# Optimization experiments

Hardware: AMD Instinct MI355X
Metric: run time of the kernel (lower is better)

The kernel has to match this reference:

```python
import jax, jax.numpy as jnp
import numpy as np

N_HEADS = 16
DIM = 1024
BS, SLEN = 2, 2048
EPS = 1e-12  # F.normalize eps


def setup_inputs() -> dict:
    key = jax.random.key(0)
    ks = jax.random.split(key, 10)
    d = DIM
    inp = {
        "x": jax.random.normal(ks[0], (BS, SLEN, d), dtype=jnp.float32),
        # causal attention mask, as produced by get_masks(causal=True)
        "mask": jnp.tril(jnp.ones((SLEN, SLEN), dtype=bool))[None].repeat(BS, axis=0),
        "Wq": jax.random.normal(ks[1], (d, d), dtype=jnp.float32) / np.sqrt(d),
        "bq": jax.random.normal(ks[2], (d,), dtype=jnp.float32) * 0.02,
        "Wk": jax.random.normal(ks[3], (d, d), dtype=jnp.float32) / np.sqrt(d),
        "bk": jax.random.normal(ks[4], (d,), dtype=jnp.float32) * 0.02,
        "Wv": jax.random.normal(ks[5], (d, d), dtype=jnp.float32) / np.sqrt(d),
        "bv": jax.random.normal(ks[6], (d,), dtype=jnp.float32) * 0.02,
        "Wo": jax.random.normal(ks[7], (d, d), dtype=jnp.float32) / np.sqrt(d),
        "bo": jax.random.normal(ks[8], (d,), dtype=jnp.float32) * 0.02,
        # learnable scale for normalized (cosine) attention
        "attention_scale": jnp.ones((1,), dtype=jnp.float32) / np.sqrt(d // N_HEADS),
    }
    return inp


def _shape(t, bs, h, dph):
    # (bs, len, dim) -> (bs, h, len, dph)
    return t.reshape(bs, -1, h, dph).transpose(0, 2, 1, 3)


def reference(x, mask, Wq, bq, Wk, bk, Wv, bv, Wo, bo, attention_scale):
    bs, qlen, dim = x.shape
    h = N_HEADS
    dph = dim // h

    q = _shape(x @ Wq + bq, bs, h, dph)  # (bs, h, qlen, dph)
    k = _shape(x @ Wk + bk, bs, h, dph)
    v = _shape(x @ Wv + bv, bs, h, dph)

    # normalized (cosine) attention: L2-normalize q and k, learned scale
    q = q / jnp.maximum(jnp.linalg.norm(q, axis=-1, keepdims=True), EPS)
    k = k / jnp.maximum(jnp.linalg.norm(k, axis=-1, keepdims=True), EPS)
    q = q * attention_scale

    scores = jnp.einsum("bhqd,bhkd->bhqk", q, k)  # (bs, h, qlen, klen)
    scores = jnp.where(mask[:, None, :, :], scores, -jnp.inf)
    weights = jax.nn.softmax(scores, axis=-1)

    ctx = jnp.einsum("bhqk,bhkd->bhqd", weights, v)
    ctx = ctx.transpose(0, 2, 1, 3).reshape(bs, qlen, dim)
    return ctx @ Wo + bo
```

## Files before the change

### kernel.cpp

```cpp
#include <hip/hip_runtime.h>
#include <math.h>

#define NH 16
#define DPH 64
#define SLEN 2048
#define BSZ 2
#define DIM 1024
#define NTOK (BSZ * SLEN)
#define LOG2E 1.44269504088896f

typedef unsigned short ushortT;
typedef __attribute__((ext_vector_type(8))) short short8;
typedef __attribute__((ext_vector_type(4))) float f32x4;

typedef __attribute__((address_space(1))) const unsigned int gu32c;
typedef __attribute__((address_space(3))) unsigned int lu32;

__device__ __forceinline__ void gld16(const void* g, void* l) {
    __builtin_amdgcn_global_load_lds((gu32c*)g, (lu32*)l, 16, 0, 0);
}

__device__ __forceinline__ ushortT f2bf(float f) {
    unsigned int u = __builtin_bit_cast(unsigned int, f);
    u = u + 0x7fffu + ((u >> 16) & 1u);
    return (ushortT)(u >> 16);
}

__device__ __forceinline__ unsigned int cvtpk_bf16(float a, float b) {
    unsigned int r;
    asm("v_cvt_pk_bf16_f32 %0, %1, %2" : "=v"(r) : "v"(a), "v"(b));
    return r;
}

__global__ __launch_bounds__(256) void cvt_all(const float* __restrict__ x,
                                               ushortT* __restrict__ xb,
                                               const float* __restrict__ W0, const float* __restrict__ W1,
                                               const float* __restrict__ W2, const float* __restrict__ W3,
                                               ushortT* __restrict__ T0, ushortT* __restrict__ T1,
                                               ushortT* __restrict__ T2, ushortT* __restrict__ T3) {
    __shared__ float tile[64][65];
    const int tid = threadIdx.x;
    const int bid = blockIdx.x;
    if (bid < 2048) {
        size_t i = (size_t)bid * 256 + tid;
        float4 a = *(const float4*)&x[i * 8];
        float4 b = *(const float4*)&x[i * 8 + 4];
        short8 v;
        v[0] = (short)f2bf(a.x); v[1] = (short)f2bf(a.y);
        v[2] = (short)f2bf(a.z); v[3] = (short)f2bf(a.w);
        v[4] = (short)f2bf(b.x); v[5] = (short)f2bf(b.y);
        v[6] = (short)f2bf(b.z); v[7] = (short)f2bf(b.w);
        *(short8*)&xb[i * 8] = v;
        return;
    }
    const int widx = bid - 2048;
    const int z = widx >> 8, rem = widx & 255;
    const float* W = z == 0 ? W0 : z == 1 ? W1 : z == 2 ? W2 : W3;
    ushortT* T = z == 0 ? T0 : z == 1 ? T1 : z == 2 ? T2 : T3;
    const int kb = (rem >> 4) * 64, nb = (rem & 15) * 64;
#pragma unroll
    for (int it = 0; it < 4; it++) {
        int chunk = it * 256 + tid;
        int r = chunk >> 4, c4 = (chunk & 15) * 4;
        *(float4*)&tile[r][c4] = *(const float4*)&W[(size_t)(kb + r) * DIM + nb + c4];
    }
    __syncthreads();
#pragma unroll
    for (int it = 0; it < 2; it++) {
        int chunk = it * 256 + tid;
        int n = chunk >> 3, k8 = (chunk & 7) * 8;
        short8 o;
#pragma unroll
        for (int j = 0; j < 8; j++) o[j] = (short)f2bf(tile[k8 + j][n]);
        *(short8*)&T[(size_t)(nb + n) * DIM + kb + k8] = o;
    }
}

__global__ __launch_bounds__(1024, 4) void gemm_qkv8(const ushortT* __restrict__ A,
                                                     const ushortT* __restrict__ Bt,
                                                     const float* __restrict__ bq,
                                                     const float* __restrict__ bk,
                                                     const float* __restrict__ bv,
                                                     const float* __restrict__ ascale,
                                                     ushortT* __restrict__ Qb,
                                                     ushortT* __restrict__ Kb,
                                                     ushortT* __restrict__ VF) {
    __shared__ __align__(16) ushortT lds[65536];
    const int tid = threadIdx.x;
    const int lane = tid & 63, wid = tid >> 6;
    const int wm = wid >> 2, wn = wid & 3;
    const int lo = lane & 15, hi = lane >> 4;
    const int bid = blockIdx.x;
    const int swz = (bid & 7) * 24 + (bid >> 3);
    const int bx = swz % 12, by = swz / 12;
    const int row0 = by * 256, col0 = bx * 256;
    const int srow = tid >> 2, sc = tid & 3;
    f32x4 acc[4][4] = {};
    short8 af[4], bfr[4];

    auto stage = [&](int isA, int buf, int ksh, int kt) {
        const ushortT* g = isA ? A : Bt;
        int r0 = isA ? row0 : col0;
        int base = (isA ? 0 : 32768) + (buf * 2 + ksh) * 8192;
        int gch = sc ^ ((srow >> 1) & 3);
        gld16(&g[(size_t)(r0 + srow) * DIM + kt * 64 + ksh * 32 + gch * 8],
              &lds[base + tid * 8]);
    };
    auto loadA = [&](int buf, int ks) {
        int base = (buf * 2 + ks) * 8192;
#pragma unroll
        for (int mm = 0; mm < 4; mm++) {
            int row = wm * 64 + mm * 16 + lo;
            af[mm] = *(const short8*)&lds[base + row * 32 + (hi ^ ((row >> 1) & 3)) * 8];
        }
    };
    auto loadB = [&](int buf, int ks) {
        int base = 32768 + (buf * 2 + ks) * 8192;
#pragma unroll
        for (int n = 0; n < 4; n++) {
            int row = wn * 64 + n * 16 + lo;
            bfr[n] = *(const short8*)&lds[base + row * 32 + (hi ^ ((row >> 1) & 3)) * 8];
        }
    };
    auto mfma16 = [&]() {
        __builtin_amdgcn_s_setprio(1);
#pragma unroll
        for (int mm = 0; mm < 4; mm++)
#pragma unroll
            for (int n = 0; n < 4; n++)
                acc[mm][n] = __builtin_amdgcn_mfma_f32_16x16x32_bf16(
                    af[mm], bfr[n], acc[mm][n], 0, 0, 0);
        __builtin_amdgcn_s_setprio(0);
    };

    stage(0, 0, 0, 0); stage(1, 0, 0, 0);
    stage(0, 0, 1, 0); stage(1, 0, 1, 0);

#pragma unroll 1
    for (int t = 0; t < 16; ++t) {
        const int cur = t & 1, nxt = cur ^ 1;
        const bool more = (t < 15);
        asm volatile("s_waitcnt vmcnt(0)" ::: "memory");
        asm volatile("s_barrier" ::: "memory");
        loadA(cur, 0); loadB(cur, 0);
        if (more) { stage(0, nxt, 0, t + 1); stage(1, nxt, 0, t + 1); }
        mfma16();
        loadA(cur, 1); loadB(cur, 1);
        if (more) { stage(0, nxt, 1, t + 1); stage(1, nxt, 1, t + 1); }
        mfma16();
    }
    __syncthreads();

    const int cg = col0 + wn * 64;
    const int which = cg >> 10;
    const int cwin = cg & 1023;
    const int h = cwin >> 6;
    const int t0g = row0 + wm * 64;
    const int b = t0g >> 11, tok0 = t0g & (SLEN - 1);
    const float* bias = which == 0 ? bq : which == 1 ? bk : bv;

    float bb4[4];
#pragma unroll
    for (int n = 0; n < 4; n++) bb4[n] = bias[cwin + n * 16 + lo];
#pragma unroll
    for (int m = 0; m < 4; m++)
#pragma unroll
        for (int n = 0; n < 4; n++)
#pragma unroll
            for (int r = 0; r < 4; r++) acc[m][n][r] += bb4[n];

    if (which < 2) {
        float asc = (which == 0) ? ascale[0] * LOG2E : 1.0f;
#pragma unroll
        for (int m = 0; m < 4; m++)
#pragma unroll
            for (int r = 0; r < 4; r++) {
                float ss = acc[m][0][r] * acc[m][0][r] + acc[m][1][r] * acc[m][1][r] +
                           acc[m][2][r] * acc[m][2][r] + acc[m][3][r] * acc[m][3][r];
#pragma unroll
                for (int o = 8; o > 0; o >>= 1) ss += __shfl_xor(ss, o);
                float sc2 = asc / fmaxf(sqrtf(ss), 1e-12f);
#pragma unroll
                for (int n = 0; n < 4; n++) acc[m][n][r] *= sc2;
            }
    }

    ushortT* tl = &lds[wid * 4096];
    if (which < 2) {
#pragma unroll
        for (int m = 0; m < 4; m++)
#pragma unroll
            for (int n = 0; n < 4; n++)
#pragma unroll
                for (int r = 0; r < 4; r++) {
                    int row = m * 16 + 4 * hi + r;
                    int c = n * 2 + (lo >> 3);
                    tl[row * 64 + ((c ^ (row & 7)) << 3) + (lo & 7)] = f2bf(acc[m][n][r]);
                }
        ushortT* op = which == 0 ? Qb : Kb;
        const size_t base = ((size_t)(b * NH + h) * SLEN + tok0) * DPH;
#pragma unroll
        for (int j = 0; j < 8; j++) {
            int cid = j * 64 + lane;
            int rowL = cid >> 3, c = cid & 7;
            uint4 v = *(const uint4*)&tl[rowL * 64 + ((c ^ (rowL & 7)) << 3)];
            *(uint4*)&op[base + (size_t)cid * 8] = v;
        }
    } else {
#pragma unroll
        for (int m = 0; m < 4; m++)
#pragma unroll
            for (int n = 0; n < 4; n++)
#pragma unroll
                for (int r = 0; r < 4; r++) {
                    int row = m * 16 + 4 * hi + r;
                    int c = n * 2 + (lo >> 3);
                    tl[row * 64 + ((c ^ ((row >> 3) & 7)) << 3) + (lo & 7)] = f2bf(acc[m][n][r]);
                }
        const int bh = b * NH + h;
        const int kt = tok0 >> 6;
#pragma unroll
        for (int c2i = 0; c2i < 8; c2i++) {
            int jd = c2i >> 1, ks2 = c2i & 1;
            int colL = jd * 16 + lo;
            int cc2 = colL >> 3;
            short8 v;
#pragma unroll
            for (int e = 0; e < 8; e++) {
                int rowL = ks2 * 32 + 8 * hi + e;
                v[e] = (short)tl[rowL * 64 + ((cc2 ^ ((rowL >> 3) & 7)) << 3) + (colL & 7)];
            }
            *(short8*)&VF[((size_t)bh * 32 + kt) * 4096 + (size_t)(c2i * 64 + lane) * 8] = v;
        }
    }
}

__global__ __launch_bounds__(512, 2) void gemm_oproj(const ushortT* __restrict__ A,
                                                     const ushortT* __restrict__ Bt,
                                                     const float* __restrict__ bias,
                                                     float* __restrict__ outF) {
    __shared__ __align__(16) ushortT lds[32768];
    const int tid = threadIdx.x;
    const int lane = tid & 63, wid = tid >> 6;
    const int wm = wid >> 2, wn = wid & 3;
    const int lo = lane & 15, hi = lane >> 4;
    const int bid = blockIdx.x;
    const int swz = (bid & 7) * 32 + (bid >> 3);
    const int bx = swz & 7, by = swz >> 3;
    const int row0 = by * 128, col0 = bx * 128;
    const int srow = tid >> 2, sc = tid & 3;
    f32x4 acc[4][2] = {};
    short8 afO[2], bfO[2];

    auto stage = [&](int isA, int buf, int ksh, int kt) {
        const ushortT* g = isA ? A : Bt;
        int r0 = isA ? row0 : col0;
        int base = (isA ? 0 : 16384) + (buf * 2 + ksh) * 4096;
        int gch = sc ^ ((srow >> 1) & 3);
        gld16(&g[(size_t)(r0 + srow) * DIM + kt * 64 + ksh * 32 + gch * 8],
              &lds[base + tid * 8]);
    };
    auto loadAO = [&](int buf, int ks, int mh) {
        int base = (buf * 2 + ks) * 4096;
#pragma unroll
        for (int mm = 0; mm < 2; mm++) {
            int row = wm * 64 + (mh * 2 + mm) * 16 + lo;
            afO[mm] = *(const short8*)&lds[base + row * 32 + (hi ^ ((row >> 1) & 3)) * 8];
        }
    };
    auto loadBO = [&](int buf, int ks) {
        int base = 16384 + (buf * 2 + ks) * 4096;
#pragma unroll
        for (int n = 0; n < 2; n++) {
            int row = wn * 32 + n * 16 + lo;
            bfO[n] = *(const short8*)&lds[base + row * 32 + (hi ^ ((row >> 1) & 3)) * 8];
        }
    };
    auto mfma4 = [&](int mh) {
        __builtin_amdgcn_s_setprio(1);
#pragma unroll
        for (int mm = 0; mm < 2; mm++)
#pragma unroll
            for (int n = 0; n < 2; n++)
                acc[mh * 2 + mm][n] = __builtin_amdgcn_mfma_f32_16x16x32_bf16(
                    afO[mm], bfO[n], acc[mh * 2 + mm][n], 0, 0, 0);
        __builtin_amdgcn_s_setprio(0);
    };

    stage(1, 0, 0, 0); stage(0, 0, 0, 0);
    stage(1, 0, 1, 0); stage(0, 0, 1, 0);
    stage(1, 1, 0, 1); stage(0, 1, 0, 1);

#pragma unroll 1
    for (int it = 0; it < 8; ++it) {
        const int o = it * 2 + 1;
        const bool more = (it < 7);
        asm volatile("s_waitcnt vmcnt(4)" ::: "memory");
        asm volatile("s_barrier" ::: "memory");
        loadAO(0, 0, 0); loadBO(0, 0);
        stage(1, 1, 1, o);
        mfma4(0);
        asm volatile("s_barrier" ::: "memory");
        loadAO(0, 0, 1);
        stage(0, 1, 1, o);
        mfma4(1);
        asm volatile("s_waitcnt vmcnt(4)" ::: "memory");
        asm volatile("s_barrier" ::: "memory");
        loadAO(0, 1, 0); loadBO(0, 1);
        if (more) stage(1, 0, 0, o + 1);
        mfma4(0);
        asm volatile("s_barrier" ::: "memory");
        loadAO(0, 1, 1);
        if (more) stage(0, 0, 0, o + 1);
        mfma4(1);
        if (more) { asm volatile("s_waitcnt vmcnt(4)" ::: "memory"); }
        else      { asm volatile("s_waitcnt vmcnt(2)" ::: "memory"); }
        asm volatile("s_barrier" ::: "memory");
        loadAO(1, 0, 0); loadBO(1, 0);
        if (more) stage(1, 0, 1, o + 1);
        mfma4(0);
        asm volatile("s_barrier" ::: "memory");
        loadAO(1, 0, 1);
        if (more) stage(0, 0, 1, o + 1);
        mfma4(1);
        if (more) { asm volatile("s_waitcnt vmcnt(4)" ::: "memory"); }
        else      { asm volatile("s_waitcnt vmcnt(0)" ::: "memory"); }
        asm volatile("s_barrier" ::: "memory");
        loadAO(1, 1, 0); loadBO(1, 1);
        if (more) stage(1, 1, 0, o + 2);
        mfma4(0);
        asm volatile("s_barrier" ::: "memory");
        loadAO(1, 1, 1);
        if (more) stage(0, 1, 0, o + 2);
        mfma4(1);
    }
    __syncthreads();

    float bb[2];
#pragma unroll
    for (int n = 0; n < 2; n++) bb[n] = bias[col0 + wn * 32 + n * 16 + lo];
#pragma unroll
    for (int m = 0; m < 4; m++)
#pragma unroll
        for (int n = 0; n < 2; n++)
#pragma unroll
            for (int r = 0; r < 4; r++) acc[m][n][r] += bb[n];

    float* tl = (float*)&lds[wid * 4096];
#pragma unroll
    for (int m = 0; m < 4; m++)
#pragma unroll
        for (int n = 0; n < 2; n++)
#pragma unroll
            for (int r = 0; r < 4; r++) {
                int row = m * 16 + hi * 4 + r;
                int col = n * 16 + lo;
                int cc = col >> 2;
                tl[row * 32 + ((cc ^ (row & 7)) << 2) + (col & 3)] = acc[m][n][r];
            }
#pragma unroll
    for (int j = 0; j < 8; j++) {
        int cid = j * 64 + lane;
        int rowR = cid >> 3, cc = cid & 7;
        f32x4 v = *(const f32x4*)&tl[rowR * 32 + ((cc ^ (rowR & 7)) << 2)];
        int rg = row0 + wm * 64 + rowR;
        int cgl = col0 + wn * 32 + cc * 4;
        *(f32x4*)&outF[(size_t)rg * DIM + cgl] = v;
    }
}

__global__ __launch_bounds__(512, 4) void attn(const ushortT* __restrict__ Q,
                                               const ushortT* __restrict__ K,
                                               const ushortT* __restrict__ VF,
                                               const float* __restrict__ scale,
                                               ushortT* __restrict__ ctx) {
    __shared__ __align__(16) ushortT Ks[2][64 * 64];
    __shared__ __align__(16) ushortT Ps[8 * 16 * 64];
    const int tid = threadIdx.x, lane = tid & 63, wid = tid >> 6;
    const int wg = wid & 3, sg = wid >> 2;
    const int bh = blockIdx.x, p = blockIdx.y;
    const int qt = sg ? p : 31 - p;
    const int kbmax = 31 - p;
    const size_t hb = (size_t)bh * SLEN * DPH;
    const int lo = lane & 15, hi = lane >> 4;
    const float mshift = fabsf(scale[0]) * LOG2E;

    short8 aq[2];
    {
        const int qrow = qt * 64 + wg * 16 + lo;
#pragma unroll
        for (int ks = 0; ks < 2; ks++)
            aq[ks] = *(const short8*)&Q[hb + (size_t)qrow * DPH + ks * 32 + 8 * hi];
    }

    const int srow = tid >> 3, sslot = tid & 7;
    const int sldsoff = srow * 64 + ((sslot ^ (srow & 7)) << 3);
    uint4 kr = *(const uint4*)&K[hb + (size_t)srow * DPH + sslot * 8];
    *(uint4*)&Ks[0][sldsoff] = kr;
    __syncthreads();

    f32x4 accd[4] = {};
    float lp = 0.f;

    for (int kb = 0; kb <= kbmax; kb++) {
        const int cur = kb & 1;
        if (kb < kbmax)
            kr = *(const uint4*)&K[hb + (size_t)((kb + 1) * 64 + srow) * DPH + sslot * 8];

        if (kb <= qt) {
            short8 bv[8];
            const ushortT* vt = &VF[(((size_t)bh * 32 + kb) * 512 + lane) * 8];
#pragma unroll
            for (int c = 0; c < 8; c++) bv[c] = *(const short8*)&vt[(size_t)c * 512];

            f32x4 sf[4] = {};
            __builtin_amdgcn_s_setprio(1);
#pragma unroll
            for (int ks = 0; ks < 2; ks++)
#pragma unroll
                for (int j = 0; j < 4; j++) {
                    int row = j * 16 + lo;
                    short8 bk = *(const short8*)&Ks[cur][row * 64 + (((ks * 4 + hi) ^ (row & 7)) << 3)];
                    sf[j] = __builtin_amdgcn_mfma_f32_16x16x32_bf16(bk, aq[ks], sf[j], 0, 0, 0);
                }
            __builtin_amdgcn_s_setprio(0);

            if (kb == qt) {
#pragma unroll
                for (int j = 0; j < 4; j++)
#pragma unroll
                    for (int r = 0; r < 4; r++)
                        if (j * 16 + 4 * hi + r > wg * 16 + lo) sf[j][r] = -INFINITY;
            }

#pragma unroll
            for (int j = 0; j < 4; j++) {
                float pv0 = __builtin_amdgcn_exp2f(sf[j][0] - mshift);
                float pv1 = __builtin_amdgcn_exp2f(sf[j][1] - mshift);
                float pv2 = __builtin_amdgcn_exp2f(sf[j][2] - mshift);
                float pv3 = __builtin_amdgcn_exp2f(sf[j][3] - mshift);
                lp += (pv0 + pv1) + (pv2 + pv3);
                uint2 pk;
                pk.x = cvtpk_bf16(pv0, pv1);
                pk.y = cvtpk_bf16(pv2, pv3);
                int slot = (4 * j + hi) ^ (2 * (lo & 7));
                *(uint2*)&Ps[wid * 1024 + lo * 64 + slot * 4] = pk;
            }

            __builtin_amdgcn_s_setprio(1);
#pragma unroll
            for (int ks = 0; ks < 2; ks++) {
                int slot0 = (8 * ks + 2 * hi) ^ (2 * (lo & 7));
                short8 ap = *(const short8*)&Ps[wid * 1024 + lo * 64 + slot0 * 4];
#pragma unroll
                for (int jd = 0; jd < 4; jd++)
                    accd[jd] = __builtin_amdgcn_mfma_f32_16x16x32_bf16(ap, bv[jd * 2 + ks], accd[jd], 0, 0, 0);
            }
            __builtin_amdgcn_s_setprio(0);
        }

        if (kb < kbmax) *(uint4*)&Ks[cur ^ 1][sldsoff] = kr;
        __syncthreads();
    }

    lp += __shfl_xor(lp, 16);
    lp += __shfl_xor(lp, 32);

    const int b = bh >> 4, h = bh & 15;
#pragma unroll
    for (int r = 0; r < 4; r++) {
        float lr = __shfl(lp, (lane & 48) | (4 * hi + r));
        float inv = 1.0f / lr;
        int t = qt * 64 + wg * 16 + 4 * hi + r;
#pragma unroll
        for (int jd = 0; jd < 4; jd++) {
            int d = jd * 16 + lo;
            ctx[(size_t)(b * SLEN + t) * DIM + h * 64 + d] = f2bf(accd[jd][r] * inv);
        }
    }
}

extern "C" void kernel_launch(void* const* d_in, const int* in_sizes, int n_in,
                              void* d_out, int out_size, void* d_ws,
                              size_t ws_size, hipStream_t stream) {
    const float* x = (const float*)d_in[0];
    const float* Wq = (const float*)d_in[2];
    const float* bq = (const float*)d_in[3];
    const float* Wk = (const float*)d_in[4];
    const float* bk = (const float*)d_in[5];
    const float* Wv = (const float*)d_in[6];
    const float* bv = (const float*)d_in[7];
    const float* Wo = (const float*)d_in[8];
    const float* bo = (const float*)d_in[9];
    const float* ascale = (const float*)d_in[10];
    float* outF = (float*)d_out;

    unsigned char* ws = (unsigned char*)d_ws;
    const size_t MB = 1u << 20;
    ushortT* xb = (ushortT*)(ws);
    ushortT* Wqkvt = (ushortT*)(ws + 8 * MB);
    ushortT* Wot = (ushortT*)(ws + 14 * MB);
    ushortT* Qb = (ushortT*)(ws + 16 * MB);
    ushortT* Kb = (ushortT*)(ws + 24 * MB);
    ushortT* VFb = (ushortT*)(ws + 32 * MB);
    ushortT* ctxb = (ushortT*)(ws + 40 * MB);

    cvt_all<<<3072, 256, 0, stream>>>(x, xb, Wq, Wk, Wv, Wo, Wqkvt,
                                      Wqkvt + (size_t)1024 * 1024,
                                      Wqkvt + (size_t)2048 * 1024, Wot);

    gemm_qkv8<<<dim3(192), 1024, 0, stream>>>(xb, Wqkvt, bq, bk, bv, ascale, Qb, Kb, VFb);

    attn<<<dim3(32, 16), 512, 0, stream>>>(Qb, Kb, VFb, ascale, ctxb);

    gemm_oproj<<<dim3(256), 512, 0, stream>>>(ctxb, Wot, bo, outF);
}
```

Measured before the change: 91.42 us.

## Simplify oproj GEMM to double-buffered loop and rebalance attention tile pairing

```diff
diff --git a/kernel.cpp b/kernel.cpp
--- a/kernel.cpp
+++ b/kernel.cpp
@@ -287,51 +287,24 @@
         __builtin_amdgcn_s_setprio(0);
     };
 
-    stage(1, 0, 0, 0); stage(0, 0, 0, 0);
-    stage(1, 0, 1, 0); stage(0, 0, 1, 0);
-    stage(1, 1, 0, 1); stage(0, 1, 0, 1);
+    stage(0, 0, 0, 0); stage(1, 0, 0, 0);
+    stage(0, 0, 1, 0); stage(1, 0, 1, 0);
 
 #pragma unroll 1
-    for (int it = 0; it < 8; ++it) {
-        const int o = it * 2 + 1;
-        const bool more = (it < 7);
-        asm volatile("s_waitcnt vmcnt(4)" ::: "memory");
+    for (int t = 0; t < 16; ++t) {
+        const int cur = t & 1, nxt = cur ^ 1;
+        const bool more = (t < 15);
+        asm volatile("s_waitcnt vmcnt(0)" ::: "memory");
         asm volatile("s_barrier" ::: "memory");
-        loadAO(0, 0, 0); loadBO(0, 0);
-        stage(1, 1, 1, o);
+        loadAO(cur, 0, 0); loadBO(cur, 0);
+        if (more) { stage(0, nxt, 0, t + 1); stage(1, nxt, 0, t + 1); }
         mfma4(0);
-        asm volatile("s_barrier" ::: "memory");
-        loadAO(0, 0, 1);
-        stage(0, 1, 1, o);
+        loadAO(cur, 0, 1);
         mfma4(1);
-        asm volatile("s_waitcnt vmcnt(4)" ::: "memory");
-        asm volatile("s_barrier" ::: "memory");
-        loadAO(0, 1, 0); loadBO(0, 1);
-        if (more) stage(1, 0, 0, o + 1);
+        loadAO(cur, 1, 0); loadBO(cur, 1);
+        if (more) { stage(0, nxt, 1, t + 1); stage(1, nxt, 1, t + 1); }
         mfma4(0);
-        asm volatile("s_barrier" ::: "memory");
-        loadAO(0, 1, 1);
-        if (more) stage(0, 0, 0, o + 1);
-        mfma4(1);
-        if (more) { asm volatile("s_waitcnt vmcnt(4)" ::: "memory"); }
-        else      { asm volatile("s_waitcnt vmcnt(2)" ::: "memory"); }
-        asm volatile("s_barrier" ::: "memory");
-        loadAO(1, 0, 0); loadBO(1, 0);
-        if (more) stage(1, 0, 1, o + 1);
-        mfma4(0);
-        asm volatile("s_barrier" ::: "memory");
-        loadAO(1, 0, 1);
-        if (more) stage(0, 0, 1, o + 1);
-        mfma4(1);
-        if (more) { asm volatile("s_waitcnt vmcnt(4)" ::: "memory"); }
-        else      { asm volatile("s_waitcnt vmcnt(0)" ::: "memory"); }
-        asm volatile("s_barrier" ::: "memory");
-        loadAO(1, 1, 0); loadBO(1, 1);
-        if (more) stage(1, 1, 0, o + 2);
-        mfma4(0);
-        asm volatile("s_barrier" ::: "memory");
-        loadAO(1, 1, 1);
-        if (more) stage(0, 1, 0, o + 2);
+        loadAO(cur, 1, 1);
         mfma4(1);
     }
     __syncthreads();
@@ -378,9 +351,11 @@
     __shared__ __align__(16) ushortT Ps[8 * 16 * 64];
     const int tid = threadIdx.x, lane = tid & 63, wid = tid >> 6;
     const int wg = wid & 3, sg = wid >> 2;
-    const int bh = blockIdx.x, p = blockIdx.y;
-    const int qt = sg ? p : 31 - p;
-    const int kbmax = 31 - p;
+    const int bid = blockIdx.x;
+    const int tp = (bid < 256) ? (15 - (bid >> 5)) : ((bid - 256) >> 5);
+    const int bh = bid & 31;
+    const int qt = 2 * tp + sg;
+    const int kbmax = 2 * tp + 1;
     const size_t hb = (size_t)bh * SLEN * DPH;
     const int lo = lane & 15, hi = lane >> 4;
     const float mshift = fabsf(scale[0]) * LOG2E;
@@ -511,7 +486,7 @@
 
     gemm_qkv8<<<dim3(192), 1024, 0, stream>>>(xb, Wqkvt, bq, bk, bv, ascale, Qb, Kb, VFb);
 
-    attn<<<dim3(32, 16), 512, 0, stream>>>(Qb, Kb, VFb, ascale, ctxb);
+    attn<<<dim3(512), 512, 0, stream>>>(Qb, Kb, VFb, ascale, ctxb);
 
     gemm_oproj<<<dim3(256), 512, 0, stream>>>(ctxb, Wot, bo, outF);
 }
```

Measured after the change: 97.74 us. +6.9%, slower.

## Pre-swizzle activations into MFMA fragment layout and load A directly from global

Applied to the files above, without the earlier changes.

```diff
diff --git a/kernel.cpp b/kernel.cpp
--- a/kernel.cpp
+++ b/kernel.cpp
@@ -33,7 +33,7 @@
 }
 
 __global__ __launch_bounds__(256) void cvt_all(const float* __restrict__ x,
-                                               ushortT* __restrict__ xb,
+                                               ushortT* __restrict__ AF,
                                                const float* __restrict__ W0, const float* __restrict__ W1,
                                                const float* __restrict__ W2, const float* __restrict__ W3,
                                                ushortT* __restrict__ T0, ushortT* __restrict__ T1,
@@ -41,19 +41,31 @@
     __shared__ float tile[64][65];
     const int tid = threadIdx.x;
     const int bid = blockIdx.x;
-    if (bid < 2048) {
-        size_t i = (size_t)bid * 256 + tid;
-        float4 a = *(const float4*)&x[i * 8];
-        float4 b = *(const float4*)&x[i * 8 + 4];
-        short8 v;
-        v[0] = (short)f2bf(a.x); v[1] = (short)f2bf(a.y);
-        v[2] = (short)f2bf(a.z); v[3] = (short)f2bf(a.w);
-        v[4] = (short)f2bf(b.x); v[5] = (short)f2bf(b.y);
-        v[6] = (short)f2bf(b.z); v[7] = (short)f2bf(b.w);
-        *(short8*)&xb[i * 8] = v;
+    if (bid < 1024) {
+        const int rt = bid >> 4, kt = bid & 15;
+#pragma unroll
+        for (int it = 0; it < 4; it++) {
+            int chunk = it * 256 + tid;
+            int r = chunk >> 4, c4 = (chunk & 15) * 4;
+            *(float4*)&tile[r][c4] =
+                *(const float4*)&x[(size_t)(rt * 64 + r) * DIM + kt * 64 + c4];
+        }
+        __syncthreads();
+#pragma unroll
+        for (int it = 0; it < 2; it++) {
+            int idx = it * 256 + tid;
+            int c = idx >> 6, l = idx & 63;
+            int mm = c >> 1, ks = c & 1;
+            int rowL = mm * 16 + (l & 15);
+            int colL = ks * 32 + (l >> 4) * 8;
+            short8 o;
+#pragma unroll
+            for (int e = 0; e < 8; e++) o[e] = (short)f2bf(tile[rowL][colL + e]);
+            *(short8*)&AF[(((size_t)rt * 16 + kt) * 8 + c) * 512 + (size_t)l * 8] = o;
+        }
         return;
     }
-    const int widx = bid - 2048;
+    const int widx = bid - 1024;
     const int z = widx >> 8, rem = widx & 255;
     const float* W = z == 0 ? W0 : z == 1 ? W1 : z == 2 ? W2 : W3;
     ushortT* T = z == 0 ? T0 : z == 1 ? T1 : z == 2 ? T2 : T3;
@@ -76,7 +88,7 @@
     }
 }
 
-__global__ __launch_bounds__(1024, 4) void gemm_qkv8(const ushortT* __restrict__ A,
+__global__ __launch_bounds__(1024, 4) void gemm_qkv8(const ushortT* __restrict__ AF,
                                                      const ushortT* __restrict__ Bt,
                                                      const float* __restrict__ bq,
                                                      const float* __restrict__ bk,
@@ -95,34 +107,33 @@
     const int bx = swz % 12, by = swz / 12;
     const int row0 = by * 256, col0 = bx * 256;
     const int srow = tid >> 2, sc = tid & 3;
+    const int rt = by * 4 + wm;
     f32x4 acc[4][4] = {};
-    short8 af[4], bfr[4];
-
-    auto stage = [&](int isA, int buf, int ksh, int kt) {
-        const ushortT* g = isA ? A : Bt;
-        int r0 = isA ? row0 : col0;
-        int base = (isA ? 0 : 32768) + (buf * 2 + ksh) * 8192;
+    short8 af0[4], af1[4], bfr[4];
+
+    auto stageB = [&](int buf, int ksh, int kt) {
+        int base = (buf * 2 + ksh) * 8192;
         int gch = sc ^ ((srow >> 1) & 3);
-        gld16(&g[(size_t)(r0 + srow) * DIM + kt * 64 + ksh * 32 + gch * 8],
+        gld16(&Bt[(size_t)(col0 + srow) * DIM + kt * 64 + ksh * 32 + gch * 8],
               &lds[base + tid * 8]);
     };
-    auto loadA = [&](int buf, int ks) {
+    auto loadAg = [&](int kt) {
+        const ushortT* base = &AF[(((size_t)rt * 16 + kt) * 8) * 512 + (size_t)lane * 8];
+#pragma unroll
+        for (int mm = 0; mm < 4; mm++) {
+            af0[mm] = *(const short8*)&base[(mm * 2 + 0) * 512];
+            af1[mm] = *(const short8*)&base[(mm * 2 + 1) * 512];
+        }
+    };
+    auto loadB = [&](int buf, int ks) {
         int base = (buf * 2 + ks) * 8192;
-#pragma unroll
-        for (int mm = 0; mm < 4; mm++) {
-            int row = wm * 64 + mm * 16 + lo;
-            af[mm] = *(const short8*)&lds[base + row * 32 + (hi ^ ((row >> 1) & 3)) * 8];
-        }
-    };
-    auto loadB = [&](int buf, int ks) {
-        int base = 32768 + (buf * 2 + ks) * 8192;
 #pragma unroll
         for (int n = 0; n < 4; n++) {
             int row = wn * 64 + n * 16 + lo;
             bfr[n] = *(const short8*)&lds[base + row * 32 + (hi ^ ((row >> 1) & 3)) * 8];
         }
     };
-    auto mfma16 = [&]() {
+    auto mfma16 = [&](short8* af) {
         __builtin_amdgcn_s_setprio(1);
 #pragma unroll
         for (int mm = 0; mm < 4; mm++)
@@ -133,8 +144,7 @@
         __builtin_amdgcn_s_setprio(0);
     };
 
-    stage(0, 0, 0, 0); stage(1, 0, 0, 0);
-    stage(0, 0, 1, 0); stage(1, 0, 1, 0);
+    stageB(0, 0, 0); stageB(0, 1, 0);
 
 #pragma unroll 1
     for (int t = 0; t < 16; ++t) {
@@ -142,12 +152,13 @@
         const bool more = (t < 15);
         asm volatile("s_waitcnt vmcnt(0)" ::: "memory");
         asm volatile("s_barrier" ::: "memory");
-        loadA(cur, 0); loadB(cur, 0);
-        if (more) { stage(0, nxt, 0, t + 1); stage(1, nxt, 0, t + 1); }
-        mfma16();
-        loadA(cur, 1); loadB(cur, 1);
-        if (more) { stage(0, nxt, 1, t + 1); stage(1, nxt, 1, t + 1); }
-        mfma16();
+        loadAg(t);
+        loadB(cur, 0);
+        if (more) stageB(nxt, 0, t + 1);
+        mfma16(af0);
+        loadB(cur, 1);
+        if (more) stageB(nxt, 1, t + 1);
+        mfma16(af1);
     }
     __syncthreads();
 
@@ -497,7 +508,7 @@
 
     unsigned char* ws = (unsigned char*)d_ws;
     const size_t MB = 1u << 20;
-    ushortT* xb = (ushortT*)(ws);
+    ushortT* AFb = (ushortT*)(ws);
     ushortT* Wqkvt = (ushortT*)(ws + 8 * MB);
     ushortT* Wot = (ushortT*)(ws + 14 * MB);
     ushortT* Qb = (ushortT*)(ws + 16 * MB);
@@ -505,11 +516,11 @@
     ushortT* VFb = (ushortT*)(ws + 32 * MB);
     ushortT* ctxb = (ushortT*)(ws + 40 * MB);
 
-    cvt_all<<<3072, 256, 0, stream>>>(x, xb, Wq, Wk, Wv, Wo, Wqkvt,
+    cvt_all<<<2048, 256, 0, stream>>>(x, AFb, Wq, Wk, Wv, Wo, Wqkvt,
                                       Wqkvt + (size_t)1024 * 1024,
                                       Wqkvt + (size_t)2048 * 1024, Wot);
 
-    gemm_qkv8<<<dim3(192), 1024, 0, stream>>>(xb, Wqkvt, bq, bk, bv, ascale, Qb, Kb, VFb);
+    gemm_qkv8<<<dim3(192), 1024, 0, stream>>>(AFb, Wqkvt, bq, bk, bv, ascale, Qb, Kb, VFb);
 
     attn<<<dim3(32, 16), 512, 0, stream>>>(Qb, Kb, VFb, ascale, ctxb);
 
```

New measurement: 98.21 us. 1.07x slower.
